# Kernel optimization log

Hardware: AMD Instinct MI355X
Metric: run time of the kernel (lower is better)

The kernel has to match this reference:

```python
import jax, jax.numpy as jnp
from jax import lax
import numpy as np

B, S, T = 64, 256, 256          # sentences, tokens, parser transitions per sentence
WDIMS, PDIMS = 128, 32
H = 256                          # per-direction hidden = ldims // 2
LDIMS = 2 * H
HID = 512
NRELS = 46
K, NNVECS = 3, 3
SLOTS = (K + 1) * NNVECS         # 12 gathered hidden vectors per transition
FEAT = LDIMS * SLOTS             # 6144 = hidLayer input dim
VW, VP = 40003, 53
ROUT = 2 * NRELS + 1             # 93


def _lstm(x, Wih, Whh, bih, bhh, reverse=False):
    """torch.nn.LSTMCell recurrence over seq axis. x: [B,S,D] -> h: [B,S,H]."""
    Bx = x.shape[0]
    Hh = Whh.shape[1]
    xs = jnp.swapaxes(x, 0, 1)  # [S,B,D]
    xg = xs @ Wih.T + (bih + bhh)  # precompute input gates [S,B,4H]

    def step(carry, g_in):
        h, c = carry
        g = g_in + h @ Whh.T
        i, f, gg, o = jnp.split(g, 4, axis=-1)
        i = jax.nn.sigmoid(i); f = jax.nn.sigmoid(f)
        gg = jnp.tanh(gg); o = jax.nn.sigmoid(o)
        c = f * c + i * gg
        h = o * jnp.tanh(c)
        return (h, c), h

    init = (jnp.zeros((Bx, Hh), x.dtype), jnp.zeros((Bx, Hh), x.dtype))
    _, hs = lax.scan(step, init, xg, reverse=reverse)
    return jnp.swapaxes(hs, 0, 1)  # [B,S,H], backward pass aligned to positions


def _forward(word_ids, pos_ids, feat_idx, wlookup, plookup,
             Wih1f, Whh1f, bih1f, bhh1f, Wih1b, Whh1b, bih1b, bhh1b,
             Wih2f, Whh2f, bih2f, bhh2f, Wih2b, Whh2b, bih2b, bhh2b,
             hidLayer, hidBias, outLayer, outBias,
             rhidLayer, rhidBias, routLayer, routBias):
    # token embeddings: ivec = cat(wordvec, posvec)
    ivec = jnp.concatenate([wlookup[word_ids], plookup[pos_ids]], axis=-1)  # [B,S,160]
    # first biLSTM
    f1 = _lstm(ivec, Wih1f, Whh1f, bih1f, bhh1f)
    b1 = _lstm(ivec, Wih1b, Whh1b, bih1b, bhh1b, reverse=True)
    vec1 = jnp.concatenate([f1, b1], axis=-1)  # [B,S,512]
    # second biLSTM (bibiFlag)
    f2 = _lstm(vec1, Wih2f, Whh2f, bih2f, bhh2f)
    b2 = _lstm(vec1, Wih2b, Whh2b, bih2b, bhh2b, reverse=True)
    vec = jnp.concatenate([f2, b2], axis=-1)  # [B,S,512]
    # __evaluate: concat (k+1)*nnvecs hidden vectors per transition
    bidx = jnp.arange(B)[:, None, None]
    feats = vec[bidx, feat_idx]                      # [B,T,12,512]
    feats = feats.reshape(B, T, FEAT)                # [B,T,6144]
    # unlabeled action scores: out = outLayer @ tanh(hidLayer @ input + hidBias) + outBias
    hid = jnp.tanh(jnp.einsum('btf,hf->bth', feats, hidLayer) + hidBias)
    out = jnp.einsum('bth,oh->bto', hid, outLayer) + outBias        # [B,T,3]
    # labeled relation scores
    rhid = jnp.tanh(jnp.einsum('btf,hf->bth', feats, rhidLayer) + rhidBias)
    rout = jnp.einsum('bth,oh->bto', rhid, routLayer) + routBias    # [B,T,93]
    return out, rout


def setup_inputs() -> dict:
    key = jax.random.key(0)
    ks = iter(jax.random.split(key, 40))

    def nrm(shape, scale=0.05):
        return jax.random.normal(next(ks), shape, jnp.float32) * scale

    inp = {}
    inp['word_ids'] = jax.random.randint(next(ks), (B, S), 0, VW)
    inp['pos_ids'] = jax.random.randint(next(ks), (B, S), 0, VP)
    inp['feat_idx'] = jax.random.randint(next(ks), (B, T, SLOTS), 0, S)
    inp['wlookup'] = nrm((VW, WDIMS))
    inp['plookup'] = nrm((VP, PDIMS))
    D1 = WDIMS + PDIMS
    for tag, din in (('1f', D1), ('1b', D1), ('2f', LDIMS), ('2b', LDIMS)):
        inp['Wih' + tag] = nrm((4 * H, din))
        inp['Whh' + tag] = nrm((4 * H, H))
        inp['bih' + tag] = nrm((4 * H,))
        inp['bhh' + tag] = nrm((4 * H,))
    inp['hidLayer'] = nrm((HID, FEAT), 0.02)
    inp['hidBias'] = nrm((HID,))
    inp['outLayer'] = nrm((3, HID))
    inp['outBias'] = nrm((3,))
    inp['rhidLayer'] = nrm((HID, FEAT), 0.02)
    inp['rhidBias'] = nrm((HID,))
    inp['routLayer'] = nrm((ROUT, HID))
    inp['routBias'] = nrm((ROUT,))
    return inp


def reference(word_ids, pos_ids, feat_idx, wlookup, plookup,
              Wih1f, Whh1f, bih1f, bhh1f, Wih1b, Whh1b, bih1b, bhh1b,
              Wih2f, Whh2f, bih2f, bhh2f, Wih2b, Whh2b, bih2b, bhh2b,
              hidLayer, hidBias, outLayer, outBias,
              rhidLayer, rhidBias, routLayer, routBias):
    return _forward(word_ids, pos_ids, feat_idx, wlookup, plookup,
                    Wih1f, Whh1f, bih1f, bhh1f, Wih1b, Whh1b, bih1b, bhh1b,
                    Wih2f, Whh2f, bih2f, bhh2f, Wih2b, Whh2b, bih2b, bhh2b,
                    hidLayer, hidBias, outLayer, outBias,
                    rhidLayer, rhidBias, routLayer, routBias)
```

## Files before the change

kernel.cpp:

```cpp
#include <hip/hip_runtime.h>
#include <hip/hip_fp16.h>
#include <math.h>


namespace {
constexpr int kB = 64, kS = 256, kH = 256, kG4 = 1024;
constexpr int kLD = 512;
constexpr int kTok = kB * kS;
}

typedef _Float16 h2 __attribute__((ext_vector_type(2)));
typedef _Float16 h4 __attribute__((ext_vector_type(4)));
typedef _Float16 h8 __attribute__((ext_vector_type(8)));
typedef float f4 __attribute__((ext_vector_type(4)));

#if __has_builtin(__builtin_amdgcn_fdot2)
#define USE_FDOT2 1
#else
#define USE_FDOT2 0
#endif

__device__ __forceinline__ float dot2acc(h2 w, h2 hh, float acc) {
#if USE_FDOT2
  return __builtin_amdgcn_fdot2(w, hh, acc, false);
#else
  return fmaf((float)w.x, (float)hh.x, fmaf((float)w.y, (float)hh.y, acc));
#endif
}

__device__ __forceinline__ float fastrcp(float x) {
#if __has_builtin(__builtin_amdgcn_rcpf)
  return __builtin_amdgcn_rcpf(x);
#else
  return 1.f / x;
#endif
}
__device__ __forceinline__ float sigf(float x) { return fastrcp(1.f + __expf(-x)); }
__device__ __forceinline__ float tanhfast(float x) {
  float u = __expf(2.f * x);
  return 1.f - 2.f * fastrcp(u + 1.f);
}

__device__ __forceinline__ float dppadd1(float x) {
#if __has_builtin(__builtin_amdgcn_mov_dpp)
  int y = __builtin_amdgcn_mov_dpp(__builtin_bit_cast(int, x), 0xB1, 0xF, 0xF, true);
  return x + __builtin_bit_cast(float, y);
#else
  return x + __shfl_xor(x, 1);
#endif
}

__device__ __forceinline__ void stage16(const void* g, void* lds_base, int lane) {
#if __has_builtin(__builtin_amdgcn_global_load_lds)
  (void)lane;
  __builtin_amdgcn_global_load_lds((const __attribute__((address_space(1))) void*)g,
                                   (__attribute__((address_space(3))) void*)lds_base,
                                   16, 0, 0);
#else
  *(uint4*)((char*)lds_base + lane * 16) = *(const uint4*)g;
#endif
}

__global__ void embed_h(const int* __restrict__ wid, const int* __restrict__ pid,
                        const float* __restrict__ wl, const float* __restrict__ pl,
                        _Float16* __restrict__ dst) {
  int tid = blockIdx.x * blockDim.x + threadIdx.x;
  if (tid >= kTok * 24) return;
  int tok = tid / 24, c8 = tid % 24;
  h8 o;
  if (c8 < 20) {
    const float* src = (c8 < 16) ? (wl + (size_t)wid[tok] * 128 + c8 * 8)
                                 : (pl + (size_t)pid[tok] * 32 + (c8 - 16) * 8);
    float4 v0 = *(const float4*)src;
    float4 v1 = *(const float4*)(src + 4);
    o[0] = (_Float16)v0.x; o[1] = (_Float16)v0.y;
    o[2] = (_Float16)v0.z; o[3] = (_Float16)v0.w;
    o[4] = (_Float16)v1.x; o[5] = (_Float16)v1.y;
    o[6] = (_Float16)v1.z; o[7] = (_Float16)v1.w;
  } else {
    o = (h8)(_Float16)0.f;
  }
  *(h8*)(dst + (size_t)tok * 192 + c8 * 8) = o;
}

__global__ void f2h_pad(const float* __restrict__ src, _Float16* __restrict__ dst,
                        int rows, int Kin, int Kpad) {
  int per = Kpad >> 2;
  int tid = blockIdx.x * blockDim.x + threadIdx.x;
  if (tid >= rows * per) return;
  int row = tid / per, c4 = (tid % per) << 2;
  h4 o;
  if (c4 < Kin) {
    float4 v = *(const float4*)(src + (size_t)row * Kin + c4);
    o[0] = (_Float16)v.x; o[1] = (_Float16)v.y;
    o[2] = (_Float16)v.z; o[3] = (_Float16)v.w;
  } else {
    o = (h4)(_Float16)0.f;
  }
  *(h4*)(dst + (size_t)row * Kpad + c4) = o;
}

__global__ void prep_bias(const float* __restrict__ b0, const float* __restrict__ b1,
                          const float* __restrict__ b2, const float* __restrict__ b3,
                          const float* __restrict__ b4, const float* __restrict__ b5,
                          const float* __restrict__ b6, const float* __restrict__ b7,
                          float* __restrict__ bsum) {
  int tid = blockIdx.x * blockDim.x + threadIdx.x;
  if (tid >= 4 * kG4) return;
  int grp = tid >> 10, i = tid & 1023;
  const float* x; const float* y;
  switch (grp) {
    case 0: x = b0; y = b1; break;
    case 1: x = b2; y = b3; break;
    case 2: x = b4; y = b5; break;
    default: x = b6; y = b7; break;
  }
  bsum[tid] = x[i] + y[i];
}

__global__ void concat_bias(const float* __restrict__ a, const float* __restrict__ b,
                            float* __restrict__ dst) {
  int tid = blockIdx.x * blockDim.x + threadIdx.x;
  if (tid >= kG4) return;
  dst[tid] = (tid < 512) ? a[tid] : b[tid - 512];
}

__global__ void build_w96(const float* __restrict__ outL, const float* __restrict__ outB,
                          const float* __restrict__ routL, const float* __restrict__ routB,
                          _Float16* __restrict__ w, float* __restrict__ b) {
  int tid = blockIdx.x * blockDim.x + threadIdx.x;
  if (tid >= 128 * 1024) return;
  int n = tid >> 10, k = tid & 1023;
  float v = 0.f;
  if (n < 3) { if (k < 512) v = outL[n * 512 + k]; }
  else if (n < 96) { if (k >= 512) v = routL[(size_t)(n - 3) * 512 + (k - 512)]; }
  w[tid] = (_Float16)v;
  if (k == 0) b[n] = (n < 3) ? outB[n] : (n < 96 ? routB[n - 3] : 0.f);
}

template <bool GATHER, int CMODE>
__global__ __launch_bounds__(256) void mfma_gemm(
    const _Float16* __restrict__ A, int lda,
    const _Float16* __restrict__ W,
    const float* __restrict__ bias,
    const _Float16* __restrict__ vsrc, const int* __restrict__ fidx,
    void* __restrict__ C, int K) {
  __shared__ _Float16 Asm[128 * 64];
  __shared__ _Float16 Bsm[128 * 64];
  const int tid = threadIdx.x;
  const int w = tid >> 6, l = tid & 63;
  const int wr = w >> 1, wc = w & 1;
  const int m0 = blockIdx.y * 128, n0 = blockIdx.x * 128;
  const int lrow = l & 15, lk8 = (l >> 4) << 3;
  const int stg_r = l >> 3;
  const int stg_c = (l & 7) ^ stg_r;

  f4 acc[4][4] = {};

  for (int k0 = 0; k0 < K; k0 += 64) {
#pragma unroll
    for (int ii = 0; ii < 4; ++ii) {
      const int r = w * 32 + ii * 8 + stg_r;
      const _Float16* ga;
      if (GATHER) {
        const int token = m0 + r;
        const int slot = k0 >> 9;
        const int idx = fidx[token * 12 + slot];
        ga = vsrc + ((((size_t)(token >> 8) << 8) + idx) << 9) + (k0 & 511) + (stg_c << 3);
      } else {
        ga = A + (size_t)(m0 + r) * lda + k0 + (stg_c << 3);
      }
      stage16(ga, &Asm[(size_t)(w * 32 + ii * 8) * 64], l);
      const _Float16* gb = W + (size_t)(n0 + r) * K + k0 + (stg_c << 3);
      stage16(gb, &Bsm[(size_t)(w * 32 + ii * 8) * 64], l);
    }
    __syncthreads();
#pragma unroll
    for (int kk = 0; kk < 64; kk += 32) {
      const int c0 = (kk + lk8) >> 3;
      h8 af[4], bf[4];
#pragma unroll
      for (int m = 0; m < 4; ++m) {
        const int row = wr * 64 + m * 16 + lrow;
        af[m] = *(const h8*)&Asm[row * 64 + ((c0 ^ (row & 7)) << 3)];
      }
#pragma unroll
      for (int n = 0; n < 4; ++n) {
        const int row = wc * 64 + n * 16 + lrow;
        bf[n] = *(const h8*)&Bsm[row * 64 + ((c0 ^ (row & 7)) << 3)];
      }
#pragma unroll
      for (int m = 0; m < 4; ++m)
#pragma unroll
        for (int n = 0; n < 4; ++n)
          acc[m][n] = __builtin_amdgcn_mfma_f32_16x16x32_f16(af[m], bf[n], acc[m][n], 0, 0, 0);
    }
    __syncthreads();
  }
#pragma unroll
  for (int n = 0; n < 4; ++n) {
    const int col = n0 + wc * 64 + n * 16 + lrow;
    const float bb = bias[col];
#pragma unroll
    for (int m = 0; m < 4; ++m) {
      const int rowb = m0 + wr * 64 + m * 16 + ((l >> 4) << 2);
#pragma unroll
      for (int r = 0; r < 4; ++r) {
        float v = acc[m][n][r] + bb;
        const size_t row = rowb + r;
        if (CMODE == 0) {
          ((float*)C)[row * kG4 + col] = v;
        } else if (CMODE == 1) {
          ((float*)C)[row * kG4 + ((col & 255) * 4 + (col >> 8))] = v;
        } else if (CMODE == 2) {
          ((_Float16*)C)[row * kG4 + col] = (_Float16)tanhf(v);
        } else {
          if (col < 3)       ((float*)C)[row * 3 + col] = v;
          else if (col < 96) ((float*)C)[(size_t)kTok * 3 + row * 93 + (col - 3)] = v;
        }
      }
    }
  }
}

__global__ __launch_bounds__(512, 2) void lstm_rec_kernel(
    const float* __restrict__ xg_f, const float* __restrict__ xg_b,
    const float* __restrict__ Whh_f, const float* __restrict__ Whh_b,
    _Float16* __restrict__ out ) {
  __shared__ uint4 wlds4[16 * 512];
  __shared__ __align__(16) _Float16 hbuf[2][kH];

  const int bid = blockIdx.x;
  const int dir = bid & 1;
  const int row = bid >> 1;
  const float* xg  = dir ? xg_b : xg_f;
  const float* Whh = dir ? Whh_b : Whh_f;
  const int t = threadIdx.x;
  const int c  = t >> 1;
  const int kh = t & 1;
  const int kbase = kh * 128;

  h2 wv[4][48];
#pragma unroll
  for (int g = 0; g < 4; ++g) {
    const float2* wr = (const float2*)(Whh + (size_t)(g * kH + c) * kH + kbase);
#pragma unroll
    for (int p = 0; p < 48; ++p) {
      float2 f = wr[p];
      h2 a; a.x = (_Float16)f.x; a.y = (_Float16)f.y;
      wv[g][p] = a;
    }
#pragma unroll
    for (int q = 0; q < 4; ++q) {
      unsigned u[4];
#pragma unroll
      for (int i = 0; i < 4; ++i) {
        float2 f = wr[48 + 4 * q + i];
        h2 a; a.x = (_Float16)f.x; a.y = (_Float16)f.y;
        u[i] = __builtin_bit_cast(unsigned, a);
      }
      wlds4[(g * 4 + q) * 512 + t] = make_uint4(u[0], u[1], u[2], u[3]);
    }
  }
  if (t < kH) hbuf[1][t] = (_Float16)0.f;
  float c_state = 0.f;
  __syncthreads();

  const float* xgr = xg + (size_t)(row * kS) * kG4;
  const int sstep = dir ? -1 : 1;
  int s = dir ? (kS - 1) : 0;
  float4 xv = *(const float4*)(xgr + (size_t)s * kG4 + 4 * c);

  for (int it = 0; it < kS; ++it) {
    int sn = s + sstep; sn = sn < 0 ? 0 : (sn > kS - 1 ? kS - 1 : sn);
    float4 xvn = *(const float4*)(xgr + (size_t)sn * kG4 + 4 * c);

    float a0 = kh ? 0.f : xv.x;
    float a1 = kh ? 0.f : xv.y;
    float a2 = kh ? 0.f : xv.z;
    float a3 = kh ? 0.f : xv.w;

    const uint4* hh = ((const uint4*)hbuf[(it & 1) ^ 1]) + kh * 16;
#pragma unroll
    for (int u = 0; u < 12; ++u) {
      uint4 hv = hh[u];
      h2 h0 = __builtin_bit_cast(h2, hv.x);
      h2 h1 = __builtin_bit_cast(h2, hv.y);
      h2 hx = __builtin_bit_cast(h2, hv.z);
      h2 h3 = __builtin_bit_cast(h2, hv.w);
      a0 = dot2acc(wv[0][4*u+0], h0, a0); a0 = dot2acc(wv[0][4*u+1], h1, a0);
      a0 = dot2acc(wv[0][4*u+2], hx, a0); a0 = dot2acc(wv[0][4*u+3], h3, a0);
      a1 = dot2acc(wv[1][4*u+0], h0, a1); a1 = dot2acc(wv[1][4*u+1], h1, a1);
      a1 = dot2acc(wv[1][4*u+2], hx, a1); a1 = dot2acc(wv[1][4*u+3], h3, a1);
      a2 = dot2acc(wv[2][4*u+0], h0, a2); a2 = dot2acc(wv[2][4*u+1], h1, a2);
      a2 = dot2acc(wv[2][4*u+2], hx, a2); a2 = dot2acc(wv[2][4*u+3], h3, a2);
      a3 = dot2acc(wv[3][4*u+0], h0, a3); a3 = dot2acc(wv[3][4*u+1], h1, a3);
      a3 = dot2acc(wv[3][4*u+2], hx, a3); a3 = dot2acc(wv[3][4*u+3], h3, a3);
    }
#pragma unroll
    for (int q = 0; q < 4; ++q) {
      uint4 hv = hh[12 + q];
      h2 h0 = __builtin_bit_cast(h2, hv.x);
      h2 h1 = __builtin_bit_cast(h2, hv.y);
      h2 hx = __builtin_bit_cast(h2, hv.z);
      h2 h3 = __builtin_bit_cast(h2, hv.w);
      uint4 w0 = wlds4[(0 * 4 + q) * 512 + t];
      uint4 w1 = wlds4[(1 * 4 + q) * 512 + t];
      uint4 w2 = wlds4[(2 * 4 + q) * 512 + t];
      uint4 w3 = wlds4[(3 * 4 + q) * 512 + t];
      a0 = dot2acc(__builtin_bit_cast(h2, w0.x), h0, a0);
      a0 = dot2acc(__builtin_bit_cast(h2, w0.y), h1, a0);
      a0 = dot2acc(__builtin_bit_cast(h2, w0.z), hx, a0);
      a0 = dot2acc(__builtin_bit_cast(h2, w0.w), h3, a0);
      a1 = dot2acc(__builtin_bit_cast(h2, w1.x), h0, a1);
      a1 = dot2acc(__builtin_bit_cast(h2, w1.y), h1, a1);
      a1 = dot2acc(__builtin_bit_cast(h2, w1.z), hx, a1);
      a1 = dot2acc(__builtin_bit_cast(h2, w1.w), h3, a1);
      a2 = dot2acc(__builtin_bit_cast(h2, w2.x), h0, a2);
      a2 = dot2acc(__builtin_bit_cast(h2, w2.y), h1, a2);
      a2 = dot2acc(__builtin_bit_cast(h2, w2.z), hx, a2);
      a2 = dot2acc(__builtin_bit_cast(h2, w2.w), h3, a2);
      a3 = dot2acc(__builtin_bit_cast(h2, w3.x), h0, a3);
      a3 = dot2acc(__builtin_bit_cast(h2, w3.y), h1, a3);
      a3 = dot2acc(__builtin_bit_cast(h2, w3.z), hx, a3);
      a3 = dot2acc(__builtin_bit_cast(h2, w3.w), h3, a3);
    }
    float s0 = dppadd1(a0);
    float s1 = dppadd1(a1);
    float s2 = dppadd1(a2);
    float s3 = dppadd1(a3);
    float i_ = sigf(s0);
    float f_ = sigf(s1);
    float g_ = tanhfast(s2);
    float o_ = sigf(s3);
    c_state = f_ * c_state + i_ * g_;
    float h = o_ * tanhfast(c_state);
    if (!kh) {
      hbuf[it & 1][c] = (_Float16)h;
      out[((size_t)(row * kS + s)) * kLD + dir * kH + c] = (_Float16)h;
    }
    s += sstep;
    __syncthreads();
    xv = xvn;
  }
}

extern "C" void kernel_launch(void* const* d_in, const int* in_sizes, int n_in,
                              void* d_out, int out_size, void* d_ws, size_t ws_size,
                              hipStream_t stream) {
  const int*   word_ids = (const int*)d_in[0];
  const int*   pos_ids  = (const int*)d_in[1];
  const int*   feat_idx = (const int*)d_in[2];
  const float* wlookup  = (const float*)d_in[3];
  const float* plookup  = (const float*)d_in[4];
  const float* Wih1f = (const float*)d_in[5];
  const float* Whh1f = (const float*)d_in[6];
  const float* bih1f = (const float*)d_in[7];
  const float* bhh1f = (const float*)d_in[8];
  const float* Wih1b = (const float*)d_in[9];
  const float* Whh1b = (const float*)d_in[10];
  const float* bih1b = (const float*)d_in[11];
  const float* bhh1b = (const float*)d_in[12];
  const float* Wih2f = (const float*)d_in[13];
  const float* Whh2f = (const float*)d_in[14];
  const float* bih2f = (const float*)d_in[15];
  const float* bhh2f = (const float*)d_in[16];
  const float* Wih2b = (const float*)d_in[17];
  const float* Whh2b = (const float*)d_in[18];
  const float* bih2b = (const float*)d_in[19];
  const float* bhh2b = (const float*)d_in[20];
  const float* hidLayer  = (const float*)d_in[21];
  const float* hidBias   = (const float*)d_in[22];
  const float* outLayer  = (const float*)d_in[23];
  const float* outBias   = (const float*)d_in[24];
  const float* rhidLayer = (const float*)d_in[25];
  const float* rhidBias  = (const float*)d_in[26];
  const float* routLayer = (const float*)d_in[27];
  const float* routBias  = (const float*)d_in[28];

  float* ws = (float*)d_ws;
  const size_t F_IVECH = 0;
  const size_t F_XGF   = F_IVECH + (size_t)kTok * 192 / 2;
  const size_t F_XGB   = F_XGF + (size_t)kTok * kG4;
  const size_t F_V1H   = F_XGB + (size_t)kTok * kG4;
  const size_t F_V2H   = F_V1H + (size_t)kTok * kLD / 2;
  const size_t F_WHA   = F_V2H + (size_t)kTok * kLD / 2;
  const size_t F_WHB   = F_WHA + (size_t)2 * kG4 * 192 / 2;
  const size_t F_WHID  = F_WHB + (size_t)2 * kG4 * 512 / 2;
  const size_t F_BSUM  = F_WHID + (size_t)kG4 * 6144 / 2;
  const size_t F_HB    = F_BSUM + 4 * kG4;
  const size_t F_W96   = F_HB + kG4;
  const size_t F_B96   = F_W96 + (size_t)128 * kG4 / 2;
  const size_t F_END   = F_B96 + 128;
  const size_t F_HID   = F_XGF;
  if (ws_size < F_END * sizeof(float)) return;

  _Float16* ivec_h = (_Float16*)(ws + F_IVECH);
  float*    xgs_f  = ws + F_XGF;
  float*    xgs_b  = ws + F_XGB;
  _Float16* vec1h  = (_Float16*)(ws + F_V1H);
  _Float16* vec2h  = (_Float16*)(ws + F_V2H);
  _Float16* whA    = (_Float16*)(ws + F_WHA);
  _Float16* whB    = (_Float16*)(ws + F_WHB);
  _Float16* whid   = (_Float16*)(ws + F_WHID);
  float*    bsum   = ws + F_BSUM;
  float*    hb     = ws + F_HB;
  _Float16* w96    = (_Float16*)(ws + F_W96);
  float*    b96    = ws + F_B96;
  _Float16* hidc_h = (_Float16*)(ws + F_HID);
  float*    outp   = (float*)d_out;

  prep_bias<<<16, 256, 0, stream>>>(bih1f, bhh1f, bih1b, bhh1b,
                                    bih2f, bhh2f, bih2b, bhh2b, bsum);
  concat_bias<<<4, 256, 0, stream>>>(hidBias, rhidBias, hb);
  build_w96<<<512, 256, 0, stream>>>(outLayer, outBias, routLayer, routBias, w96, b96);
  f2h_pad<<<(1024 * 48 + 255) / 256, 256, 0, stream>>>(Wih1f, whA, 1024, 160, 192);
  f2h_pad<<<(1024 * 48 + 255) / 256, 256, 0, stream>>>(Wih1b, whA + 1024 * 192, 1024, 160, 192);
  f2h_pad<<<(1024 * 128 + 255) / 256, 256, 0, stream>>>(Wih2f, whB, 1024, 512, 512);
  f2h_pad<<<(1024 * 128 + 255) / 256, 256, 0, stream>>>(Wih2b, whB + 1024 * 512, 1024, 512, 512);
  f2h_pad<<<(512 * 1536 + 255) / 256, 256, 0, stream>>>(hidLayer, whid, 512, 6144, 6144);
  f2h_pad<<<(512 * 1536 + 255) / 256, 256, 0, stream>>>(rhidLayer, whid + (size_t)512 * 6144,
                                                        512, 6144, 6144);
  embed_h<<<(kTok * 24 + 255) / 256, 256, 0, stream>>>(word_ids, pos_ids,
                                                       wlookup, plookup, ivec_h);
  mfma_gemm<false, 1><<<dim3(8, 128), 256, 0, stream>>>(
      ivec_h, 192, whA, bsum + 0, nullptr, nullptr, xgs_f, 192);
  mfma_gemm<false, 1><<<dim3(8, 128), 256, 0, stream>>>(
      ivec_h, 192, whA + 1024 * 192, bsum + 1024, nullptr, nullptr, xgs_b, 192);
  lstm_rec_kernel<<<128, 512, 0, stream>>>(xgs_f, xgs_b, Whh1f, Whh1b, vec1h);
  mfma_gemm<false, 1><<<dim3(8, 128), 256, 0, stream>>>(
      vec1h, 512, whB, bsum + 2048, nullptr, nullptr, xgs_f, 512);
  mfma_gemm<false, 1><<<dim3(8, 128), 256, 0, stream>>>(
      vec1h, 512, whB + 1024 * 512, bsum + 3072, nullptr, nullptr, xgs_b, 512);
  lstm_rec_kernel<<<128, 512, 0, stream>>>(xgs_f, xgs_b, Whh2f, Whh2b, vec2h);
  mfma_gemm<true, 2><<<dim3(8, 128), 256, 0, stream>>>(
      nullptr, 0, whid, hb, vec2h, feat_idx, hidc_h, 6144);
  mfma_gemm<false, 3><<<dim3(1, 128), 256, 0, stream>>>(
      hidc_h, kG4, w96, b96, nullptr, nullptr, outp, kG4);
}
```

Baseline: 1.641 ms.

## Add 256-row gather GEMM, rebalance LSTM weight split, swizzle LDS

Replaces the feature-gather hidden-layer GEMM with a dedicated 512-thread kernel that computes 256x128 tiles, so each B (weight) tile is reused across twice as many rows. The LSTM recurrence now keeps 52 instead of 48 weight pairs per gate in registers and 3 instead of 4 chunks in LDS, with an XOR swizzle on LDS indices to avoid bank conflicts. The x-gate load is no longer prefetched a step ahead; it is now issued at the top of each step and added after the reduction. The trade-off is higher register pressure in the recurrence and possible load latency exposed on the serial path.

```diff
diff --git a/kernel.cpp b/kernel.cpp
--- a/kernel.cpp
+++ b/kernel.cpp
@@ -208,9 +208,7 @@
       for (int r = 0; r < 4; ++r) {
         float v = acc[m][n][r] + bb;
         const size_t row = rowb + r;
-        if (CMODE == 0) {
-          ((float*)C)[row * kG4 + col] = v;
-        } else if (CMODE == 1) {
+        if (CMODE == 1) {
           ((float*)C)[row * kG4 + ((col & 255) * 4 + (col >> 8))] = v;
         } else if (CMODE == 2) {
           ((_Float16*)C)[row * kG4 + col] = (_Float16)tanhf(v);
@@ -223,11 +221,83 @@
   }
 }
 
+__global__ __launch_bounds__(512) void mfma_gemm_g256(
+    const _Float16* __restrict__ W,
+    const float* __restrict__ bias,
+    const _Float16* __restrict__ vsrc, const int* __restrict__ fidx,
+    _Float16* __restrict__ C, int K) {
+  __shared__ _Float16 Asm[256 * 64];
+  __shared__ _Float16 Bsm[128 * 64];
+  const int tid = threadIdx.x;
+  const int w = tid >> 6, l = tid & 63;
+  const int wr = w >> 1, wc = w & 1;
+  const int m0 = blockIdx.y * 256, n0 = blockIdx.x * 128;
+  const int lrow = l & 15, lk8 = (l >> 4) << 3;
+  const int stg_r = l >> 3;
+  const int stg_c = (l & 7) ^ stg_r;
+
+  f4 acc[4][4] = {};
+
+  for (int k0 = 0; k0 < K; k0 += 64) {
+#pragma unroll
+    for (int ii = 0; ii < 4; ++ii) {
+      const int token = m0 + w * 32 + ii * 8 + stg_r;
+      const int slot = k0 >> 9;
+      const int idx = fidx[token * 12 + slot];
+      const _Float16* ga =
+          vsrc + ((((size_t)(token >> 8) << 8) + idx) << 9) + (k0 & 511) + (stg_c << 3);
+      stage16(ga, &Asm[(size_t)(w * 32 + ii * 8) * 64], l);
+    }
+#pragma unroll
+    for (int ii = 0; ii < 2; ++ii) {
+      const int r = w * 16 + ii * 8 + stg_r;
+      const _Float16* gb = W + (size_t)(n0 + r) * K + k0 + (stg_c << 3);
+      stage16(gb, &Bsm[(size_t)(w * 16 + ii * 8) * 64], l);
+    }
+    __syncthreads();
+#pragma unroll
+    for (int kk = 0; kk < 64; kk += 32) {
+      const int c0 = (kk + lk8) >> 3;
+      h8 af[4], bf[4];
+#pragma unroll
+      for (int m = 0; m < 4; ++m) {
+        const int row = wr * 64 + m * 16 + lrow;
+        af[m] = *(const h8*)&Asm[row * 64 + ((c0 ^ (row & 7)) << 3)];
+      }
+#pragma unroll
+      for (int n = 0; n < 4; ++n) {
+        const int row = wc * 64 + n * 16 + lrow;
+        bf[n] = *(const h8*)&Bsm[row * 64 + ((c0 ^ (row & 7)) << 3)];
+      }
+#pragma unroll
+      for (int m = 0; m < 4; ++m)
+#pragma unroll
+        for (int n = 0; n < 4; ++n)
+          acc[m][n] = __builtin_amdgcn_mfma_f32_16x16x32_f16(af[m], bf[n], acc[m][n], 0, 0, 0);
+    }
+    __syncthreads();
+  }
+#pragma unroll
+  for (int n = 0; n < 4; ++n) {
+    const int col = n0 + wc * 64 + n * 16 + lrow;
+    const float bb = bias[col];
+#pragma unroll
+    for (int m = 0; m < 4; ++m) {
+      const int rowb = m0 + wr * 64 + m * 16 + ((l >> 4) << 2);
+#pragma unroll
+      for (int r = 0; r < 4; ++r) {
+        float v = acc[m][n][r] + bb;
+        C[(size_t)(rowb + r) * kG4 + col] = (_Float16)tanhf(v);
+      }
+    }
+  }
+}
+
 __global__ __launch_bounds__(512, 2) void lstm_rec_kernel(
     const float* __restrict__ xg_f, const float* __restrict__ xg_b,
     const float* __restrict__ Whh_f, const float* __restrict__ Whh_b,
     _Float16* __restrict__ out ) {
-  __shared__ uint4 wlds4[16 * 512];
+  __shared__ uint4 wlds4[12 * 512];
   __shared__ __align__(16) _Float16 hbuf[2][kH];
 
   const int bid = blockIdx.x;
@@ -239,27 +309,28 @@
   const int c  = t >> 1;
   const int kh = t & 1;
   const int kbase = kh * 128;
-
-  h2 wv[4][48];
+  const int tsw = t ^ ((t >> 3) & 7);
+
+  h2 wv[4][52];
 #pragma unroll
   for (int g = 0; g < 4; ++g) {
     const float2* wr = (const float2*)(Whh + (size_t)(g * kH + c) * kH + kbase);
 #pragma unroll
-    for (int p = 0; p < 48; ++p) {
+    for (int p = 0; p < 52; ++p) {
       float2 f = wr[p];
       h2 a; a.x = (_Float16)f.x; a.y = (_Float16)f.y;
       wv[g][p] = a;
     }
 #pragma unroll
-    for (int q = 0; q < 4; ++q) {
+    for (int q = 0; q < 3; ++q) {
       unsigned u[4];
 #pragma unroll
       for (int i = 0; i < 4; ++i) {
-        float2 f = wr[48 + 4 * q + i];
+        float2 f = wr[52 + 4 * q + i];
         h2 a; a.x = (_Float16)f.x; a.y = (_Float16)f.y;
         u[i] = __builtin_bit_cast(unsigned, a);
       }
-      wlds4[(g * 4 + q) * 512 + t] = make_uint4(u[0], u[1], u[2], u[3]);
+      wlds4[(g * 3 + q) * 512 + tsw] = make_uint4(u[0], u[1], u[2], u[3]);
     }
   }
   if (t < kH) hbuf[1][t] = (_Float16)0.f;
@@ -269,20 +340,14 @@
   const float* xgr = xg + (size_t)(row * kS) * kG4;
   const int sstep = dir ? -1 : 1;
   int s = dir ? (kS - 1) : 0;
-  float4 xv = *(const float4*)(xgr + (size_t)s * kG4 + 4 * c);
 
   for (int it = 0; it < kS; ++it) {
-    int sn = s + sstep; sn = sn < 0 ? 0 : (sn > kS - 1 ? kS - 1 : sn);
-    float4 xvn = *(const float4*)(xgr + (size_t)sn * kG4 + 4 * c);
-
-    float a0 = kh ? 0.f : xv.x;
-    float a1 = kh ? 0.f : xv.y;
-    float a2 = kh ? 0.f : xv.z;
-    float a3 = kh ? 0.f : xv.w;
-
+    const float4 xv = *(const float4*)(xgr + (size_t)s * kG4 + 4 * c);
+
+    float a0 = 0.f, a1 = 0.f, a2 = 0.f, a3 = 0.f;
     const uint4* hh = ((const uint4*)hbuf[(it & 1) ^ 1]) + kh * 16;
 #pragma unroll
-    for (int u = 0; u < 12; ++u) {
+    for (int u = 0; u < 13; ++u) {
       uint4 hv = hh[u];
       h2 h0 = __builtin_bit_cast(h2, hv.x);
       h2 h1 = __builtin_bit_cast(h2, hv.y);
@@ -298,16 +363,16 @@
       a3 = dot2acc(wv[3][4*u+2], hx, a3); a3 = dot2acc(wv[3][4*u+3], h3, a3);
     }
 #pragma unroll
-    for (int q = 0; q < 4; ++q) {
-      uint4 hv = hh[12 + q];
+    for (int q = 0; q < 3; ++q) {
+      uint4 hv = hh[13 + q];
       h2 h0 = __builtin_bit_cast(h2, hv.x);
       h2 h1 = __builtin_bit_cast(h2, hv.y);
       h2 hx = __builtin_bit_cast(h2, hv.z);
       h2 h3 = __builtin_bit_cast(h2, hv.w);
-      uint4 w0 = wlds4[(0 * 4 + q) * 512 + t];
-      uint4 w1 = wlds4[(1 * 4 + q) * 512 + t];
-      uint4 w2 = wlds4[(2 * 4 + q) * 512 + t];
-      uint4 w3 = wlds4[(3 * 4 + q) * 512 + t];
+      uint4 w0 = wlds4[(0 * 3 + q) * 512 + tsw];
+      uint4 w1 = wlds4[(1 * 3 + q) * 512 + tsw];
+      uint4 w2 = wlds4[(2 * 3 + q) * 512 + tsw];
+      uint4 w3 = wlds4[(3 * 3 + q) * 512 + tsw];
       a0 = dot2acc(__builtin_bit_cast(h2, w0.x), h0, a0);
       a0 = dot2acc(__builtin_bit_cast(h2, w0.y), h1, a0);
       a0 = dot2acc(__builtin_bit_cast(h2, w0.z), hx, a0);
@@ -325,10 +390,10 @@
       a3 = dot2acc(__builtin_bit_cast(h2, w3.z), hx, a3);
       a3 = dot2acc(__builtin_bit_cast(h2, w3.w), h3, a3);
     }
-    float s0 = dppadd1(a0);
-    float s1 = dppadd1(a1);
-    float s2 = dppadd1(a2);
-    float s3 = dppadd1(a3);
+    float s0 = dppadd1(a0) + xv.x;
+    float s1 = dppadd1(a1) + xv.y;
+    float s2 = dppadd1(a2) + xv.z;
+    float s3 = dppadd1(a3) + xv.w;
     float i_ = sigf(s0);
     float f_ = sigf(s1);
     float g_ = tanhfast(s2);
@@ -341,7 +406,6 @@
     }
     s += sstep;
     __syncthreads();
-    xv = xvn;
   }
 }
 
@@ -433,8 +497,8 @@
   mfma_gemm<false, 1><<<dim3(8, 128), 256, 0, stream>>>(
       vec1h, 512, whB + 1024 * 512, bsum + 3072, nullptr, nullptr, xgs_b, 512);
   lstm_rec_kernel<<<128, 512, 0, stream>>>(xgs_f, xgs_b, Whh2f, Whh2b, vec2h);
-  mfma_gemm<true, 2><<<dim3(8, 128), 256, 0, stream>>>(
-      nullptr, 0, whid, hb, vec2h, feat_idx, hidc_h, 6144);
+  mfma_gemm_g256<<<dim3(8, 64), 512, 0, stream>>>(
+      whid, hb, vec2h, feat_idx, hidc_h, 6144);
   mfma_gemm<false, 3><<<dim3(1, 128), 256, 0, stream>>>(
       hidc_h, kG4, w96, b96, nullptr, nullptr, outp, kG4);
 }
```

New measurement: 1.531 ms. 6.7% less time.
